# Kernel tuning notes

Measured on AMD Instinct MI355X. Metric: run time of the kernel, lower is better.

Reference implementation:

```python
import jax, jax.numpy as jnp
import numpy as np

EPS = 1e-6  # nn.CosineSimilarity eps


def setup_inputs() -> dict:
    key = jax.random.key(0)
    k1, k2, k3, k4, k5 = jax.random.split(key, 5)
    V1, V2, D = 50000, 100000, 768
    LQ, T, N = 32, 131072, 8192
    table1 = jax.random.normal(k1, (V1, D), dtype=jnp.float32)
    table2 = jax.random.normal(k2, (V2, D), dtype=jnp.float32)
    q_ids = jax.random.randint(k3, (LQ,), 0, V1, dtype=jnp.int64)
    cand_ids = jax.random.randint(k4, (T,), 0, V2, dtype=jnp.int64)
    cand_segments = jnp.sort(jax.random.randint(k5, (T,), 0, N, dtype=jnp.int64))
    return {
        "table1": table1,
        "table2": table2,
        "q_ids": q_ids,
        "cand_ids": cand_ids,
        "cand_segments": cand_segments,
        "num_candidates": N,
    }


def reference(table1, table2, q_ids, cand_ids, cand_segments, num_candidates):
    # sequence_embedding for the query: mean of gathered token vectors  [D]
    q_emb = jnp.mean(table1[q_ids], axis=0)

    # sequence_embedding for every recipe2 candidate via segment mean  [N, D]
    gathered = table2[cand_ids]  # [T, D]
    sums = jax.ops.segment_sum(gathered, cand_segments, num_segments=num_candidates)
    counts = jax.ops.segment_sum(
        jnp.ones((cand_ids.shape[0],), dtype=table2.dtype),
        cand_segments,
        num_segments=num_candidates,
    )
    # empty candidate -> zero embedding (len(node)==0 branch)
    cand_emb = sums / jnp.maximum(counts, 1.0)[:, None]

    # cosine similarity (torch clamps each norm by eps)
    q_norm = jnp.maximum(jnp.linalg.norm(q_emb), EPS)
    c_norm = jnp.maximum(jnp.linalg.norm(cand_emb, axis=1), EPS)
    cos = (cand_emb @ q_emb) / (q_norm * c_norm)  # [N]
    return cos[None, :]
```

## Files before the change

kernel.cpp:

```cpp
#include <hip/hip_runtime.h>

#define DD 768
#define NT 192
#define EPSF 1e-6f

__device__ inline float wave_reduce_sum(float v) {
    #pragma unroll
    for (int off = 32; off > 0; off >>= 1)
        v += __shfl_down(v, off, 64);
    return v;
}

__global__ void __launch_bounds__(NT) qemb_kernel(const float* __restrict__ table1,
                                                  const int* __restrict__ q_ids,
                                                  int LQ,
                                                  float* __restrict__ ws) {
    int tid = threadIdx.x;
    float4 acc = make_float4(0.f, 0.f, 0.f, 0.f);
    for (int i = 0; i < LQ; ++i) {
        const float4* row = reinterpret_cast<const float4*>(table1 + (long long)q_ids[i] * DD);
        float4 v = row[tid];
        acc.x += v.x; acc.y += v.y; acc.z += v.z; acc.w += v.w;
    }
    float inv = 1.0f / (float)LQ;
    acc.x *= inv; acc.y *= inv; acc.z *= inv; acc.w *= inv;
    reinterpret_cast<float4*>(ws)[tid] = acc;

    float n2 = acc.x * acc.x + acc.y * acc.y + acc.z * acc.z + acc.w * acc.w;
    n2 = wave_reduce_sum(n2);
    __shared__ float part[3];
    int wid = tid >> 6;
    if ((tid & 63) == 0) part[wid] = n2;
    __syncthreads();
    if (tid == 0) {
        float t = part[0] + part[1] + part[2];
        ws[DD] = fmaxf(sqrtf(t), EPSF);
    }
}

__global__ void __launch_bounds__(NT) segcos_kernel(const float* __restrict__ table2,
                                                    const int* __restrict__ cand_ids,
                                                    const int* __restrict__ segs,
                                                    int T,
                                                    const float* __restrict__ ws,
                                                    float* __restrict__ out) {
    int n = blockIdx.x;
    int tid = threadIdx.x;

    int lo, hi;
    {
        int l = 0, r = T;
        while (l < r) { int m = (l + r) >> 1; if (segs[m] < n) l = m + 1; else r = m; }
        lo = l;
        r = T;
        while (l < r) { int m = (l + r) >> 1; if (segs[m] <= n) l = m + 1; else r = m; }
        hi = l;
    }

    float4 q = reinterpret_cast<const float4*>(ws)[tid];
    float qn = ws[DD];

    float4 acc = make_float4(0.f, 0.f, 0.f, 0.f);
    for (int i = lo; i < hi; ++i) {
        const float4* row = reinterpret_cast<const float4*>(table2 + (long long)cand_ids[i] * DD);
        float4 v = row[tid];
        acc.x += v.x; acc.y += v.y; acc.z += v.z; acc.w += v.w;
    }

    float dot = acc.x * q.x + acc.y * q.y + acc.z * q.z + acc.w * q.w;
    float n2  = acc.x * acc.x + acc.y * acc.y + acc.z * acc.z + acc.w * acc.w;
    dot = wave_reduce_sum(dot);
    n2  = wave_reduce_sum(n2);

    __shared__ float pd[3], pn[3];
    int wid = tid >> 6;
    if ((tid & 63) == 0) { pd[wid] = dot; pn[wid] = n2; }
    __syncthreads();
    if (tid == 0) {
        float sdot = pd[0] + pd[1] + pd[2];
        float sn2  = pn[0] + pn[1] + pn[2];
        float cnt  = (float)(hi - lo);
        float c    = fmaxf(cnt, 1.0f);
        float cd   = sdot / c;
        float cn   = fmaxf(sqrtf(sn2) / c, EPSF);
        out[n] = cd / (qn * cn);
    }
}

extern "C" void kernel_launch(void* const* d_in, const int* in_sizes, int n_in,
                              void* d_out, int out_size, void* d_ws, size_t ws_size,
                              hipStream_t stream) {
    const float* table1   = (const float*)d_in[0];
    const float* table2   = (const float*)d_in[1];
    const int*   q_ids    = (const int*)d_in[2];
    const int*   cand_ids = (const int*)d_in[3];
    const int*   segs     = (const int*)d_in[4];

    int LQ = in_sizes[2];
    int T  = in_sizes[3];
    int N  = out_size;

    float* ws  = (float*)d_ws;
    float* out = (float*)d_out;

    qemb_kernel<<<1, NT, 0, stream>>>(table1, q_ids, LQ, ws);
    segcos_kernel<<<N, NT, 0, stream>>>(table2, cand_ids, segs, T, ws, out);
}
```

Measured before the change: 482.3 us.

## Precompute segment starts and assign one wavefront per candidate with unrolled gathers

Replaces the per-block double binary search over the segment array with a separate kernel that writes segment start offsets, so each candidate reads its range directly. The main kernel now gives each 64-lane wavefront one candidate, with each lane covering three float4 slices, and unrolls the gather loop by two rows for more loads in flight. This drops the shared-memory cross-wave reduction and __syncthreads. It adds one kernel launch and a workspace array of starts placed at a fixed offset in the workspace.

```diff
diff --git a/kernel.cpp b/kernel.cpp
--- a/kernel.cpp
+++ b/kernel.cpp
@@ -1,20 +1,12 @@
 #include <hip/hip_runtime.h>
 
 #define DD 768
-#define NT 192
 #define EPSF 1e-6f
 
-__device__ inline float wave_reduce_sum(float v) {
-    #pragma unroll
-    for (int off = 32; off > 0; off >>= 1)
-        v += __shfl_down(v, off, 64);
-    return v;
-}
-
-__global__ void __launch_bounds__(NT) qemb_kernel(const float* __restrict__ table1,
-                                                  const int* __restrict__ q_ids,
-                                                  int LQ,
-                                                  float* __restrict__ ws) {
+__global__ void __launch_bounds__(192) qemb_kernel(const float* __restrict__ table1,
+                                                   const int* __restrict__ q_ids,
+                                                   int LQ,
+                                                   float* __restrict__ ws) {
     int tid = threadIdx.x;
     float4 acc = make_float4(0.f, 0.f, 0.f, 0.f);
     for (int i = 0; i < LQ; ++i) {
@@ -27,7 +19,8 @@
     reinterpret_cast<float4*>(ws)[tid] = acc;
 
     float n2 = acc.x * acc.x + acc.y * acc.y + acc.z * acc.z + acc.w * acc.w;
-    n2 = wave_reduce_sum(n2);
+    #pragma unroll
+    for (int off = 32; off > 0; off >>= 1) n2 += __shfl_down(n2, off, 64);
     __shared__ float part[3];
     int wid = tid >> 6;
     if ((tid & 63) == 0) part[wid] = n2;
@@ -38,52 +31,74 @@
     }
 }
 
-__global__ void __launch_bounds__(NT) segcos_kernel(const float* __restrict__ table2,
-                                                    const int* __restrict__ cand_ids,
-                                                    const int* __restrict__ segs,
-                                                    int T,
-                                                    const float* __restrict__ ws,
-                                                    float* __restrict__ out) {
-    int n = blockIdx.x;
-    int tid = threadIdx.x;
+__global__ void __launch_bounds__(256) starts_kernel(const int* __restrict__ segs,
+                                                     int T, int N,
+                                                     int* __restrict__ starts) {
+    int i = blockIdx.x * blockDim.x + threadIdx.x;
+    if (i > T) return;
+    int prev = (i > 0) ? segs[i - 1] : -1;
+    int cur  = (i < T) ? segs[i]     : N;
+    for (int n = prev + 1; n <= cur; ++n) starts[n] = i;
+}
 
-    int lo, hi;
-    {
-        int l = 0, r = T;
-        while (l < r) { int m = (l + r) >> 1; if (segs[m] < n) l = m + 1; else r = m; }
-        lo = l;
-        r = T;
-        while (l < r) { int m = (l + r) >> 1; if (segs[m] <= n) l = m + 1; else r = m; }
-        hi = l;
+#define ACC4(A, V) do { A.x += V.x; A.y += V.y; A.z += V.z; A.w += V.w; } while (0)
+
+__global__ void __launch_bounds__(256) segcos_kernel(const float* __restrict__ table2,
+                                                     const int* __restrict__ cand_ids,
+                                                     const int* __restrict__ starts,
+                                                     const float* __restrict__ ws,
+                                                     float* __restrict__ out,
+                                                     int N) {
+    int tid  = threadIdx.x;
+    int lane = tid & 63;
+    int n    = blockIdx.x * 4 + (tid >> 6);
+    if (n >= N) return;
+
+    int lo = starts[n];
+    int hi = starts[n + 1];
+
+    const float4* Q = reinterpret_cast<const float4*>(ws);
+    float4 q0 = Q[lane], q1 = Q[lane + 64], q2 = Q[lane + 128];
+    float  qn = ws[DD];
+
+    float4 a0 = make_float4(0.f,0.f,0.f,0.f);
+    float4 a1 = make_float4(0.f,0.f,0.f,0.f);
+    float4 a2 = make_float4(0.f,0.f,0.f,0.f);
+
+    int i = lo;
+    for (; i + 2 <= hi; i += 2) {
+        long long id0 = cand_ids[i];
+        long long id1 = cand_ids[i + 1];
+        const float4* r0 = reinterpret_cast<const float4*>(table2 + id0 * DD);
+        const float4* r1 = reinterpret_cast<const float4*>(table2 + id1 * DD);
+        float4 x0 = r0[lane], x1 = r0[lane + 64], x2 = r0[lane + 128];
+        float4 y0 = r1[lane], y1 = r1[lane + 64], y2 = r1[lane + 128];
+        ACC4(a0, x0); ACC4(a1, x1); ACC4(a2, x2);
+        ACC4(a0, y0); ACC4(a1, y1); ACC4(a2, y2);
+    }
+    if (i < hi) {
+        long long id0 = cand_ids[i];
+        const float4* r0 = reinterpret_cast<const float4*>(table2 + id0 * DD);
+        float4 x0 = r0[lane], x1 = r0[lane + 64], x2 = r0[lane + 128];
+        ACC4(a0, x0); ACC4(a1, x1); ACC4(a2, x2);
     }
 
-    float4 q = reinterpret_cast<const float4*>(ws)[tid];
-    float qn = ws[DD];
-
-    float4 acc = make_float4(0.f, 0.f, 0.f, 0.f);
-    for (int i = lo; i < hi; ++i) {
-        const float4* row = reinterpret_cast<const float4*>(table2 + (long long)cand_ids[i] * DD);
-        float4 v = row[tid];
-        acc.x += v.x; acc.y += v.y; acc.z += v.z; acc.w += v.w;
+    float dot = a0.x*q0.x + a0.y*q0.y + a0.z*q0.z + a0.w*q0.w
+              + a1.x*q1.x + a1.y*q1.y + a1.z*q1.z + a1.w*q1.w
+              + a2.x*q2.x + a2.y*q2.y + a2.z*q2.z + a2.w*q2.w;
+    float n2  = a0.x*a0.x + a0.y*a0.y + a0.z*a0.z + a0.w*a0.w
+              + a1.x*a1.x + a1.y*a1.y + a1.z*a1.z + a1.w*a1.w
+              + a2.x*a2.x + a2.y*a2.y + a2.z*a2.z + a2.w*a2.w;
+    #pragma unroll
+    for (int off = 32; off > 0; off >>= 1) {
+        dot += __shfl_down(dot, off, 64);
+        n2  += __shfl_down(n2,  off, 64);
     }
-
-    float dot = acc.x * q.x + acc.y * q.y + acc.z * q.z + acc.w * q.w;
-    float n2  = acc.x * acc.x + acc.y * acc.y + acc.z * acc.z + acc.w * acc.w;
-    dot = wave_reduce_sum(dot);
-    n2  = wave_reduce_sum(n2);
-
-    __shared__ float pd[3], pn[3];
-    int wid = tid >> 6;
-    if ((tid & 63) == 0) { pd[wid] = dot; pn[wid] = n2; }
-    __syncthreads();
-    if (tid == 0) {
-        float sdot = pd[0] + pd[1] + pd[2];
-        float sn2  = pn[0] + pn[1] + pn[2];
-        float cnt  = (float)(hi - lo);
-        float c    = fmaxf(cnt, 1.0f);
-        float cd   = sdot / c;
-        float cn   = fmaxf(sqrtf(sn2) / c, EPSF);
-        out[n] = cd / (qn * cn);
+    if (lane == 0) {
+        float cnt = (float)(hi - lo);
+        float c   = fmaxf(cnt, 1.0f);
+        float cn  = fmaxf(sqrtf(n2) / c, EPSF);
+        out[n] = (dot / c) / (qn * cn);
     }
 }
 
@@ -100,9 +115,11 @@
     int T  = in_sizes[3];
     int N  = out_size;
 
-    float* ws  = (float*)d_ws;
-    float* out = (float*)d_out;
+    float* ws     = (float*)d_ws;
+    int*   starts = (int*)((char*)d_ws + 4096);
+    float* out    = (float*)d_out;
 
-    qemb_kernel<<<1, NT, 0, stream>>>(table1, q_ids, LQ, ws);
-    segcos_kernel<<<N, NT, 0, stream>>>(table2, cand_ids, segs, T, ws, out);
+    qemb_kernel<<<1, 192, 0, stream>>>(table1, q_ids, LQ, ws);
+    starts_kernel<<<(T + 1 + 255) / 256, 256, 0, stream>>>(segs, T, N, starts);
+    segcos_kernel<<<(N + 3) / 4, 256, 0, stream>>>(table2, cand_ids, starts, ws, out, N);
 }
```

After: 478.2 us. About the same (-0.9%).
